# Kernel tuning notes

Hardware: AMD Instinct MI355X
Metric: run time of the kernel (lower is better)

Reference implementation:

```python
import jax, jax.numpy as jnp
import numpy as np
import math

B = 8
LATENT = 1024
K_DIM = 128   # conv input channels / view dim k
M_DIM = 256   # attention feature dim m
N = 4096      # points_num // num_branch; attention seq len
EPS = 1e-5


def _bn(h, g, b, m, v):
    # inference-mode BatchNorm1d over [B, C, L]
    return (h - m[None, :, None]) * (g / jnp.sqrt(v + EPS))[None, :, None] + b[None, :, None]


def _conv(h, w, b):
    # Conv1d with kernel_size=1 == channel matmul: h [B,C,L], w [O,C]
    return jnp.einsum('bcl,oc->bol', h, w) + b[None, :, None]


def setup_inputs() -> dict:
    key = jax.random.key(0)
    ks = jax.random.split(key, 64)
    it = iter(range(64))

    def nrm(shape, scale=0.05):
        return jax.random.normal(ks[next(it)], shape, jnp.float32) * scale

    def pos(shape):
        return jax.random.uniform(ks[next(it)], shape, jnp.float32, 0.5, 1.5)

    d = {}
    d['x'] = jax.random.normal(ks[next(it)], (B, LATENT), jnp.float32)
    d['fc1_w'] = nrm((M_DIM * K_DIM, LATENT))
    d['fc1_b'] = nrm((M_DIM * K_DIM,))
    d['c1q_w'] = nrm((64, K_DIM)); d['c1q_b'] = nrm((64,))
    d['c2q_w'] = nrm((128, 64));   d['c2q_b'] = nrm((128,))
    d['c3q_w'] = nrm((N, 128));    d['c3q_b'] = nrm((N,))
    d['c3k_w'] = nrm((N, 128));    d['c3k_b'] = nrm((N,))
    d['c1v_w'] = nrm((64, K_DIM)); d['c1v_b'] = nrm((64,))
    d['c2v_w'] = nrm((128, 64));   d['c2v_b'] = nrm((128,))
    d['c3v_w'] = nrm((N, 128));    d['c3v_b'] = nrm((N,))
    for nm, c in [('bn1q', 64), ('bn2q', 128), ('bn1k', 64), ('bn2k', 128), ('bn1v', 64), ('bn2v', 128)]:
        d[nm + '_g'] = pos((c,))
        d[nm + '_be'] = nrm((c,))
        d[nm + '_m'] = nrm((c,))
        d[nm + '_v'] = pos((c,))
    d['co_w'] = nrm((3, M_DIM)); d['co_b'] = nrm((3,))
    return d


def _forward(x, fc1_w, fc1_b, c1q_w, c1q_b, c2q_w, c2q_b, c3q_w, c3q_b, c3k_w, c3k_b,
             c1v_w, c1v_b, c2v_w, c2v_b, c3v_w, c3v_b,
             bn1q_g, bn1q_be, bn1q_m, bn1q_v, bn2q_g, bn2q_be, bn2q_m, bn2q_v,
             bn1k_g, bn1k_be, bn1k_m, bn1k_v, bn2k_g, bn2k_be, bn2k_m, bn2k_v,
             bn1v_g, bn1v_be, bn1v_m, bn1v_v, bn2v_g, bn2v_be, bn2v_m, bn2v_v,
             co_w, co_b):
    h = (x @ fc1_w.T + fc1_b).reshape(-1, M_DIM, K_DIM)   # [B, m, k]
    h = jnp.transpose(h, (0, 2, 1))                        # [B, k, m]
    # Q path
    Q = jax.nn.relu(_bn(_conv(h, c1q_w, c1q_b), bn1q_g, bn1q_be, bn1q_m, bn1q_v))
    Q = jax.nn.relu(_bn(_conv(Q, c2q_w, c2q_b), bn2q_g, bn2q_be, bn2q_m, bn2q_v))
    Q = _conv(Q, c3q_w, c3q_b)                             # [B, n, m]
    # K path: source re-uses conv1_q / conv2_q weights (faithful to original)
    K = jax.nn.relu(_bn(_conv(h, c1q_w, c1q_b), bn1k_g, bn1k_be, bn1k_m, bn1k_v))
    K = jax.nn.relu(_bn(_conv(K, c2q_w, c2q_b), bn2k_g, bn2k_be, bn2k_m, bn2k_v))
    K = _conv(K, c3k_w, c3k_b)                             # [B, n, m]
    # V path
    V = jax.nn.relu(_bn(_conv(h, c1v_w, c1v_b), bn1v_g, bn1v_be, bn1v_m, bn1v_v))
    V = jax.nn.relu(_bn(_conv(V, c2v_w, c2v_b), bn2v_g, bn2v_be, bn2v_m, bn2v_v))
    V = _conv(V, c3v_w, c3v_b)                             # [B, n, m]
    # hand-rolled attention: scores [B, n, n] (source scales by sqrt(k))
    scores = jnp.einsum('bim,bjm->bij', Q, K) / math.sqrt(K_DIM)
    attn = jax.nn.softmax(scores, axis=2)
    out = jnp.einsum('bij,bjm->bim', attn, V)              # [B, n, m]
    out = jnp.einsum('bnm,om->bon', out, co_w) + co_b[None, :, None]  # [B, 3, n]
    return jnp.transpose(out, (0, 2, 1))                   # [B, n, 3]


def reference(x, fc1_w, fc1_b, c1q_w, c1q_b, c2q_w, c2q_b, c3q_w, c3q_b, c3k_w, c3k_b,
              c1v_w, c1v_b, c2v_w, c2v_b, c3v_w, c3v_b,
              bn1q_g, bn1q_be, bn1q_m, bn1q_v, bn2q_g, bn2q_be, bn2q_m, bn2q_v,
              bn1k_g, bn1k_be, bn1k_m, bn1k_v, bn2k_g, bn2k_be, bn2k_m, bn2k_v,
              bn1v_g, bn1v_be, bn1v_m, bn1v_v, bn2v_g, bn2v_be, bn2v_m, bn2v_v,
              co_w, co_b):
    return _forward(x, fc1_w, fc1_b, c1q_w, c1q_b, c2q_w, c2q_b, c3q_w, c3q_b, c3k_w, c3k_b,
                    c1v_w, c1v_b, c2v_w, c2v_b, c3v_w, c3v_b,
                    bn1q_g, bn1q_be, bn1q_m, bn1q_v, bn2q_g, bn2q_be, bn2q_m, bn2q_v,
                    bn1k_g, bn1k_be, bn1k_m, bn1k_v, bn2k_g, bn2k_be, bn2k_m, bn2k_v,
                    bn1v_g, bn1v_be, bn1v_m, bn1v_v, bn2v_g, bn2v_be, bn2v_m, bn2v_v,
                    co_w, co_b)
```

## Files before the change

### kernel.cpp

```cpp
#include <hip/hip_runtime.h>
#include <cstdint>
#include <cstddef>

#define EPS 1e-5f

typedef __attribute__((ext_vector_type(8))) short bf16x8;
typedef __attribute__((ext_vector_type(4))) float f32x4;
typedef __attribute__((ext_vector_type(16))) float f32x16;

__device__ __forceinline__ unsigned short rne_bf16(float f) {
  union { float f; unsigned int u; } v; v.f = f;
  unsigned int u = v.u;
  return (unsigned short)((u + 0x7fffu + ((u >> 16) & 1u)) >> 16);
}
__device__ __forceinline__ float bf16_to_f(unsigned short h) {
  union { unsigned int u; float f; } v; v.u = ((unsigned int)h) << 16; return v.f;
}
__device__ __forceinline__ void split_hl(float v, unsigned short& h, unsigned short& l) {
  h = rne_bf16(v);
  l = rne_bf16(v - bf16_to_f(h));
}
__device__ __forceinline__ f32x4 mfma16(bf16x8 a, bf16x8 b, f32x4 c) {
  return __builtin_amdgcn_mfma_f32_16x16x32_bf16(a, b, c, 0, 0, 0);
}
__device__ __forceinline__ f32x16 mfma32(bf16x8 a, bf16x8 b, f32x16 c) {
  return __builtin_amdgcn_mfma_f32_32x32x16_bf16(a, b, c, 0, 0, 0);
}

__global__ __launch_bounds__(256) void k_fc1(const float* __restrict__ x,
                                             const float* __restrict__ w,
                                             const float* __restrict__ bias,
                                             float* __restrict__ h_t) {
  const int lane = threadIdx.x & 63;
  const int wv = threadIdx.x >> 6;
  const int r = blockIdx.x * 4 + wv;
  const float4* wr = (const float4*)(w + (size_t)r * 1024);
  float acc[8] = {0, 0, 0, 0, 0, 0, 0, 0};
#pragma unroll
  for (int i = 0; i < 4; ++i) {
    float4 wv4 = wr[lane + i * 64];
#pragma unroll
    for (int b = 0; b < 8; ++b) {
      float4 xv = ((const float4*)(x + b * 1024))[lane + i * 64];
      acc[b] += wv4.x * xv.x + wv4.y * xv.y + wv4.z * xv.z + wv4.w * xv.w;
    }
  }
#pragma unroll
  for (int d = 1; d < 64; d <<= 1) {
#pragma unroll
    for (int b = 0; b < 8; ++b) acc[b] += __shfl_xor(acc[b], d);
  }
  if (lane == 0) {
    const int mm = r >> 7, kk = r & 127;
    const float bb = bias[r];
#pragma unroll
    for (int b = 0; b < 8; ++b) h_t[b * 32768 + kk * 256 + mm] = acc[b] + bb;
  }
}

__global__ __launch_bounds__(256) void k_conv1(
    const float* __restrict__ h_t,
    const float* __restrict__ c1q_w, const float* __restrict__ c1q_b,
    const float* __restrict__ c1v_w, const float* __restrict__ c1v_b,
    const float* __restrict__ g1q, const float* __restrict__ be1q,
    const float* __restrict__ mu1q, const float* __restrict__ va1q,
    const float* __restrict__ g1k, const float* __restrict__ be1k,
    const float* __restrict__ mu1k, const float* __restrict__ va1k,
    const float* __restrict__ g1v, const float* __restrict__ be1v,
    const float* __restrict__ mu1v, const float* __restrict__ va1v,
    float* __restrict__ T1q, float* __restrict__ T1k, float* __restrict__ T1v) {
  const int m = threadIdx.x;
  const int o = blockIdx.x & 63;
  const int b = blockIdx.x >> 6;
  const int path = blockIdx.y;
  const float* w = (path == 0 ? c1q_w : c1v_w) + o * 128;
  const float* h = h_t + b * 32768 + m;
  float acc = 0.f;
#pragma unroll 8
  for (int c = 0; c < 128; ++c) acc += w[c] * h[c * 256];
  if (path == 0) {
    const float z = acc + c1q_b[o];
    const float sq = g1q[o] / sqrtf(va1q[o] + EPS);
    T1q[b * 16384 + o * 256 + m] = fmaxf((z - mu1q[o]) * sq + be1q[o], 0.f);
    const float sk = g1k[o] / sqrtf(va1k[o] + EPS);
    T1k[b * 16384 + o * 256 + m] = fmaxf((z - mu1k[o]) * sk + be1k[o], 0.f);
  } else {
    const float z = acc + c1v_b[o];
    const float sv = g1v[o] / sqrtf(va1v[o] + EPS);
    T1v[b * 16384 + o * 256 + m] = fmaxf((z - mu1v[o]) * sv + be1v[o], 0.f);
  }
}

__global__ __launch_bounds__(256) void k_conv2(
    const float* __restrict__ T1q, const float* __restrict__ T1k,
    const float* __restrict__ T1v,
    const float* __restrict__ c2q_w, const float* __restrict__ c2q_b,
    const float* __restrict__ c2v_w, const float* __restrict__ c2v_b,
    const float* __restrict__ g2q, const float* __restrict__ be2q,
    const float* __restrict__ mu2q, const float* __restrict__ va2q,
    const float* __restrict__ g2k, const float* __restrict__ be2k,
    const float* __restrict__ mu2k, const float* __restrict__ va2k,
    const float* __restrict__ g2v, const float* __restrict__ be2v,
    const float* __restrict__ mu2v, const float* __restrict__ va2v,
    unsigned short* __restrict__ Q2H, unsigned short* __restrict__ Q2L,
    unsigned short* __restrict__ K2H, unsigned short* __restrict__ K2L,
    float* __restrict__ V2F) {
  const int m = threadIdx.x;
  const int b = blockIdx.x;
  const int path = blockIdx.y;
  const int oc = blockIdx.z;
  const float* T1 = (path == 0 ? T1q : path == 1 ? T1k : T1v) + b * 16384 + m;
  const float* w = (path == 2 ? c2v_w : c2q_w);
  const float* cb = (path == 2 ? c2v_b : c2q_b);
  const float* g = (path == 0 ? g2q : path == 1 ? g2k : g2v);
  const float* be = (path == 0 ? be2q : path == 1 ? be2k : be2v);
  const float* mu = (path == 0 ? mu2q : path == 1 ? mu2k : mu2v);
  const float* va = (path == 0 ? va2q : path == 1 ? va2k : va2v);
  float t[64];
#pragma unroll
  for (int c = 0; c < 64; ++c) t[c] = T1[c * 256];
  unsigned short* oh =
      (path == 0 ? Q2H : K2H) + b * 32768 + m * 128 + oc * 64;
  unsigned short* ol =
      (path == 0 ? Q2L : K2L) + b * 32768 + m * 128 + oc * 64;
  for (int og = 0; og < 8; ++og) {
    bf16x8 ph, pl;
#pragma unroll
    for (int j = 0; j < 8; ++j) {
      const int o = oc * 64 + og * 8 + j;
      float acc = cb[o];
      const float* wo = w + o * 64;
#pragma unroll
      for (int c = 0; c < 64; ++c) acc += wo[c] * t[c];
      const float s = g[o] / sqrtf(va[o] + EPS);
      const float val = fmaxf((acc - mu[o]) * s + be[o], 0.f);
      if (path == 2) {
        V2F[b * 32768 + o * 256 + m] = val;
      } else {
        unsigned short hh, ll;
        split_hl(val, hh, ll);
        ph[j] = (short)hh; pl[j] = (short)ll;
      }
    }
    if (path != 2) {
      *(bf16x8*)(oh + og * 8) = ph;
      *(bf16x8*)(ol + og * 8) = pl;
    }
  }
}

__global__ __launch_bounds__(256) void k_conv3all(
    const float* __restrict__ c3q_w, const float* __restrict__ c3q_b,
    const float* __restrict__ c3k_w, const float* __restrict__ c3k_b,
    const unsigned short* __restrict__ Q2H, const unsigned short* __restrict__ Q2L,
    const unsigned short* __restrict__ K2H, const unsigned short* __restrict__ K2L,
    unsigned short* __restrict__ QhB, unsigned short* __restrict__ QlB,
    unsigned short* __restrict__ KhB, unsigned short* __restrict__ KlB,
    const float* __restrict__ c3v_w, const float* __restrict__ c3v_b,
    const float* __restrict__ V2F, const float* __restrict__ co_w,
    float4* __restrict__ Vpp) {
  const int z = blockIdx.z;
  const int b = blockIdx.y;
  if (z == 2) {
    if (blockIdx.x >= 16) return;
    __shared__ float Us[387];
    __shared__ float Up[256][3];
    const int tt = threadIdx.x;
    {
      const int c = tt >> 1, mh = tt & 1;
      const float* v = V2F + b * 32768 + c * 256 + mh * 128;
      const float* cw0 = co_w + mh * 128;
      float u0 = 0.f, u1 = 0.f, u2 = 0.f;
#pragma unroll 4
      for (int mm = 0; mm < 128; ++mm) {
        const float xv = v[mm];
        u0 += xv * cw0[mm];
        u1 += xv * cw0[256 + mm];
        u2 += xv * cw0[512 + mm];
      }
      Up[tt][0] = u0; Up[tt][1] = u1; Up[tt][2] = u2;
      if (tt < 3) {
        float s = 0.f;
        for (int mm = 0; mm < 256; ++mm) s += co_w[tt * 256 + mm];
        Us[384 + tt] = s;
      }
    }
    __syncthreads();
    if ((tt & 1) == 0) {
      const int c = tt >> 1;
      Us[c * 3 + 0] = Up[tt][0] + Up[tt + 1][0];
      Us[c * 3 + 1] = Up[tt][1] + Up[tt + 1][1];
      Us[c * 3 + 2] = Up[tt][2] + Up[tt + 1][2];
    }
    __syncthreads();
    const int n = blockIdx.x * 256 + tt;
    const float* w = c3v_w + (size_t)n * 128;
    float a0 = 0.f, a1 = 0.f, a2 = 0.f;
#pragma unroll 4
    for (int c = 0; c < 128; ++c) {
      const float wc = w[c];
      a0 += wc * Us[c * 3 + 0];
      a1 += wc * Us[c * 3 + 1];
      a2 += wc * Us[c * 3 + 2];
    }
    const float bb = c3v_b[n];
    Vpp[(size_t)b * 4096 + n] =
        make_float4(a0 + bb * Us[384], a1 + bb * Us[385], a2 + bb * Us[386], 0.f);
    return;
  }
  const float* W = (z == 0) ? c3q_w : c3k_w;
  const float* bias = (z == 0) ? c3q_b : c3k_b;
  const unsigned short* Xh = (z == 0) ? Q2H : K2H;
  const unsigned short* Xl = (z == 0) ? Q2L : K2L;
  unsigned short* Yh = (z == 0) ? QhB : KhB;
  unsigned short* Yl = (z == 0) ? QlB : KlB;
  const float scale = (z == 0) ? 0.08838834764831845f * 1.4426950408889634f : 1.0f;
  const int lane = threadIdx.x & 63, wv = threadIdx.x >> 6;
  const int l15 = lane & 15, quad = lane >> 4;
  const unsigned short* XH = Xh + b * 32768;
  const unsigned short* XL = Xl + b * 32768;
  unsigned short* YH = Yh + (size_t)b * 4096 * 256;
  unsigned short* YL = Yl + (size_t)b * 4096 * 256;
  const int nb = blockIdx.x * 64 + wv * 16;
  const float* wr = W + (size_t)(nb + l15) * 128 + quad * 8;
  bf16x8 ah[4], al[4];
#pragma unroll
  for (int ks = 0; ks < 4; ++ks) {
#pragma unroll
    for (int j = 0; j < 8; ++j) {
      unsigned short hh, ll;
      split_hl(wr[ks * 32 + j], hh, ll);
      ah[ks][j] = (short)hh; al[ks][j] = (short)ll;
    }
  }
  f32x4 acc[16];
#pragma unroll
  for (int ms = 0; ms < 16; ++ms) acc[ms] = (f32x4){0, 0, 0, 0};
#pragma unroll
  for (int ks = 0; ks < 4; ++ks) {
#pragma unroll
    for (int ms = 0; ms < 16; ++ms) {
      const size_t off = (size_t)(ms * 16 + l15) * 128 + ks * 32 + quad * 8;
      bf16x8 bh = *(const bf16x8*)(XH + off);
      bf16x8 bl = *(const bf16x8*)(XL + off);
      acc[ms] = mfma16(ah[ks], bh, acc[ms]);
      acc[ms] = mfma16(al[ks], bh, acc[ms]);
      acc[ms] = mfma16(ah[ks], bl, acc[ms]);
    }
  }
#pragma unroll
  for (int r = 0; r < 4; ++r) {
    const int n = nb + quad * 4 + r;
    const float bv = bias[n];
#pragma unroll
    for (int ms = 0; ms < 16; ++ms) {
      const float v = (acc[ms][r] + bv) * scale;
      unsigned short hh, ll;
      split_hl(v, hh, ll);
      YH[(size_t)n * 256 + ms * 16 + l15] = hh;
      YL[(size_t)n * 256 + ms * 16 + l15] = ll;
    }
  }
}

__global__ __launch_bounds__(256, 2) void k_attn(
    const unsigned short* __restrict__ Qh, const unsigned short* __restrict__ Ql,
    const unsigned short* __restrict__ Kh, const unsigned short* __restrict__ Kl,
    const float4* __restrict__ Vpp, float* __restrict__ partsum,
    unsigned int* __restrict__ cnt, const float* __restrict__ co_b,
    float* __restrict__ out) {
  __shared__ __align__(16) short Kt[2][2][32 * 264];
  __shared__ __align__(16) float4 Vt[2][32];
  const int t = threadIdx.x;
  const int lane = t & 63, wv = t >> 6;
  const int l31 = lane & 31, half = lane >> 5;
  const int b = blockIdx.x & 7;
  const int qt = (blockIdx.x >> 3) & 31;
  const int jh = blockIdx.x >> 8;
  const int qrow = qt * 128 + wv * 32 + l31;
  const size_t qoff = ((size_t)b * 4096 + qrow) * 256 + half * 8;
  bf16x8 qfh[16], qfl[16];
#pragma unroll
  for (int kc = 0; kc < 16; ++kc) {
    qfh[kc] = *(const bf16x8*)(Qh + qoff + kc * 16);
    qfl[kc] = *(const bf16x8*)(Ql + qoff + kc * 16);
  }
  const unsigned short* Kgh = Kh + (size_t)b * 4096 * 256;
  const unsigned short* Kgl = Kl + (size_t)b * 4096 * 256;
  const float4* Vg = Vpp + (size_t)b * 4096;
  const int r0 = t >> 5;
  const int sseg = (t & 31) * 8;
  float a0 = 0.f, a1 = 0.f, a2 = 0.f, al = 0.f;
  const int jt0 = jh * 64;
  {
    const int jbase = jt0 * 32;
#pragma unroll
    for (int i = 0; i < 4; ++i) {
      const int row = i * 8 + r0;
      const size_t g = (size_t)(jbase + row) * 256 + sseg;
      *(bf16x8*)&Kt[0][0][row * 264 + sseg] = *(const bf16x8*)(Kgh + g);
      *(bf16x8*)&Kt[0][1][row * 264 + sseg] = *(const bf16x8*)(Kgl + g);
    }
    if (t < 32) Vt[0][t] = Vg[jbase + t];
  }
  __syncthreads();
  for (int it = 0; it < 64; ++it) {
    const int cur = it & 1, nxt = cur ^ 1;
    const bool pf = (it < 63);
    bf16x8 th[4], tl[4];
    float4 vpf = make_float4(0.f, 0.f, 0.f, 0.f);
    if (pf) {
      const int jb2 = (jt0 + it + 1) * 32;
#pragma unroll
      for (int i = 0; i < 4; ++i) {
        const size_t g = (size_t)(jb2 + i * 8 + r0) * 256 + sseg;
        th[i] = *(const bf16x8*)(Kgh + g);
        tl[i] = *(const bf16x8*)(Kgl + g);
      }
      if (t < 32) vpf = Vg[jb2 + t];
    }
    f32x16 sA, sB, sC;
#pragma unroll
    for (int r = 0; r < 16; ++r) { sA[r] = 0.f; sB[r] = 0.f; sC[r] = 0.f; }
    const short* KH = Kt[cur][0];
    const short* KL = Kt[cur][1];
    __builtin_amdgcn_s_setprio(1);
#pragma unroll
    for (int kc = 0; kc < 16; ++kc) {
      bf16x8 kh = *(const bf16x8*)&KH[l31 * 264 + kc * 16 + half * 8];
      bf16x8 kl = *(const bf16x8*)&KL[l31 * 264 + kc * 16 + half * 8];
      sA = mfma32(kh, qfh[kc], sA);
      sB = mfma32(kh, qfl[kc], sB);
      sC = mfma32(kl, qfh[kc], sC);
    }
    __builtin_amdgcn_s_setprio(0);
#pragma unroll
    for (int r = 0; r < 16; ++r) {
      const float p = __builtin_amdgcn_exp2f(sA[r] + sB[r] + sC[r]);
      const float4 vj = Vt[cur][(r & 3) + 8 * (r >> 2) + 4 * half];
      a0 += p * vj.x; a1 += p * vj.y; a2 += p * vj.z; al += p;
    }
    if (pf) {
#pragma unroll
      for (int i = 0; i < 4; ++i) {
        const int row = i * 8 + r0;
        *(bf16x8*)&Kt[nxt][0][row * 264 + sseg] = th[i];
        *(bf16x8*)&Kt[nxt][1][row * 264 + sseg] = tl[i];
      }
      if (t < 32) Vt[nxt][t] = vpf;
    }
    __syncthreads();
  }
  a0 += __shfl_xor(a0, 32);
  a1 += __shfl_xor(a1, 32);
  a2 += __shfl_xor(a2, 32);
  al += __shfl_xor(al, 32);
  if (half == 0) {
    const int idx = b * 4096 + qrow;
    float* ps = partsum + (size_t)idx * 4;
    atomicAdd(ps + 0, a0);
    atomicAdd(ps + 1, a1);
    atomicAdd(ps + 2, a2);
    atomicAdd(ps + 3, al);
    __threadfence();
    const unsigned int old = atomicAdd(&cnt[idx], 1u);
    if (old == 1u) {
      const float s0 = atomicAdd(ps + 0, 0.f);
      const float s1 = atomicAdd(ps + 1, 0.f);
      const float s2 = atomicAdd(ps + 2, 0.f);
      const float sl = atomicAdd(ps + 3, 0.f);
      const float rl = 1.f / sl;
      out[(size_t)idx * 3 + 0] = s0 * rl + co_b[0];
      out[(size_t)idx * 3 + 1] = s1 * rl + co_b[1];
      out[(size_t)idx * 3 + 2] = s2 * rl + co_b[2];
    }
  }
}

extern "C" void kernel_launch(void* const* d_in, const int* in_sizes, int n_in,
                              void* d_out, int out_size, void* d_ws, size_t ws_size,
                              hipStream_t stream) {
  const float* x = (const float*)d_in[0];
  const float* fc1_w = (const float*)d_in[1];
  const float* fc1_b = (const float*)d_in[2];
  const float* c1q_w = (const float*)d_in[3];
  const float* c1q_b = (const float*)d_in[4];
  const float* c2q_w = (const float*)d_in[5];
  const float* c2q_b = (const float*)d_in[6];
  const float* c3q_w = (const float*)d_in[7];
  const float* c3q_b = (const float*)d_in[8];
  const float* c3k_w = (const float*)d_in[9];
  const float* c3k_b = (const float*)d_in[10];
  const float* c1v_w = (const float*)d_in[11];
  const float* c1v_b = (const float*)d_in[12];
  const float* c2v_w = (const float*)d_in[13];
  const float* c2v_b = (const float*)d_in[14];
  const float* c3v_w = (const float*)d_in[15];
  const float* c3v_b = (const float*)d_in[16];
  const float* bn1q_g = (const float*)d_in[17];
  const float* bn1q_be = (const float*)d_in[18];
  const float* bn1q_m = (const float*)d_in[19];
  const float* bn1q_v = (const float*)d_in[20];
  const float* bn2q_g = (const float*)d_in[21];
  const float* bn2q_be = (const float*)d_in[22];
  const float* bn2q_m = (const float*)d_in[23];
  const float* bn2q_v = (const float*)d_in[24];
  const float* bn1k_g = (const float*)d_in[25];
  const float* bn1k_be = (const float*)d_in[26];
  const float* bn1k_m = (const float*)d_in[27];
  const float* bn1k_v = (const float*)d_in[28];
  const float* bn2k_g = (const float*)d_in[29];
  const float* bn2k_be = (const float*)d_in[30];
  const float* bn2k_m = (const float*)d_in[31];
  const float* bn2k_v = (const float*)d_in[32];
  const float* bn1v_g = (const float*)d_in[33];
  const float* bn1v_be = (const float*)d_in[34];
  const float* bn1v_m = (const float*)d_in[35];
  const float* bn1v_v = (const float*)d_in[36];
  const float* bn2v_g = (const float*)d_in[37];
  const float* bn2v_be = (const float*)d_in[38];
  const float* bn2v_m = (const float*)d_in[39];
  const float* bn2v_v = (const float*)d_in[40];
  const float* co_w = (const float*)d_in[41];
  const float* co_b = (const float*)d_in[42];

  char* ws = (char*)d_ws;
  float* h_t = (float*)(ws + 0);
  float* T1q = (float*)(ws + 1048576);
  float* T1k = (float*)(ws + 1572864);
  float* T1v = (float*)(ws + 2097152);
  unsigned short* Q2H = (unsigned short*)(ws + 2621440);
  unsigned short* Q2L = (unsigned short*)(ws + 3145728);
  unsigned short* K2H = (unsigned short*)(ws + 3670016);
  unsigned short* K2L = (unsigned short*)(ws + 4194304);
  float* V2F = (float*)(ws + 4718592);
  unsigned short* QhB = (unsigned short*)(ws + 5767168);
  unsigned short* QlB = (unsigned short*)(ws + 22544384);
  unsigned short* KhB = (unsigned short*)(ws + 39321600);
  unsigned short* KlB = (unsigned short*)(ws + 56098816);
  float4* Vpp = (float4*)(ws + 72876032);
  float* partsum = (float*)(ws + 73416704);
  unsigned int* cnt = (unsigned int*)(ws + 73940992);

  hipMemsetAsync(ws + 73416704, 0, 524288 + 131072, stream);

  k_fc1<<<8192, 256, 0, stream>>>(x, fc1_w, fc1_b, h_t);
  k_conv1<<<dim3(512, 2), 256, 0, stream>>>(
      h_t, c1q_w, c1q_b, c1v_w, c1v_b,
      bn1q_g, bn1q_be, bn1q_m, bn1q_v,
      bn1k_g, bn1k_be, bn1k_m, bn1k_v,
      bn1v_g, bn1v_be, bn1v_m, bn1v_v,
      T1q, T1k, T1v);
  k_conv2<<<dim3(8, 3, 2), 256, 0, stream>>>(
      T1q, T1k, T1v, c2q_w, c2q_b, c2v_w, c2v_b,
      bn2q_g, bn2q_be, bn2q_m, bn2q_v,
      bn2k_g, bn2k_be, bn2k_m, bn2k_v,
      bn2v_g, bn2v_be, bn2v_m, bn2v_v,
      Q2H, Q2L, K2H, K2L, V2F);
  k_conv3all<<<dim3(64, 8, 3), 256, 0, stream>>>(
      c3q_w, c3q_b, c3k_w, c3k_b, Q2H, Q2L, K2H, K2L,
      QhB, QlB, KhB, KlB, c3v_w, c3v_b, V2F, co_w, Vpp);
  k_attn<<<512, 256, 0, stream>>>(QhB, QlB, KhB, KlB, Vpp, partsum, cnt,
                                  co_b, (float*)d_out);
}
```

Before: 707.0 us.

## Process two query subtiles per wave in attention to reuse K tiles

Each wave in the attention kernel now handles 64 query rows (two 32-row subtiles) instead of 32, so every K tile loaded from LDS feeds twice as many MFMAs. The grid is halved to 256 blocks and launch bounds drop to one block per CU. LDS double buffering is replaced by a single buffer with an extra barrier before overwriting it. This raises register pressure, lowers occupancy to 256 blocks, and serialises the K tile handoff between iterations.

```diff
diff --git a/kernel.cpp b/kernel.cpp
--- a/kernel.cpp
+++ b/kernel.cpp
@@ -263,116 +263,129 @@
   }
 }
 
-__global__ __launch_bounds__(256, 2) void k_attn(
+__global__ __launch_bounds__(256, 1) void k_attn(
     const unsigned short* __restrict__ Qh, const unsigned short* __restrict__ Ql,
     const unsigned short* __restrict__ Kh, const unsigned short* __restrict__ Kl,
     const float4* __restrict__ Vpp, float* __restrict__ partsum,
     unsigned int* __restrict__ cnt, const float* __restrict__ co_b,
     float* __restrict__ out) {
-  __shared__ __align__(16) short Kt[2][2][32 * 264];
-  __shared__ __align__(16) float4 Vt[2][32];
+  __shared__ __align__(16) short Kth[32 * 264];
+  __shared__ __align__(16) short Ktl[32 * 264];
+  __shared__ __align__(16) float4 Vt[32];
   const int t = threadIdx.x;
   const int lane = t & 63, wv = t >> 6;
   const int l31 = lane & 31, half = lane >> 5;
   const int b = blockIdx.x & 7;
-  const int qt = (blockIdx.x >> 3) & 31;
-  const int jh = blockIdx.x >> 8;
-  const int qrow = qt * 128 + wv * 32 + l31;
-  const size_t qoff = ((size_t)b * 4096 + qrow) * 256 + half * 8;
-  bf16x8 qfh[16], qfl[16];
+  const int qt = (blockIdx.x >> 3) & 15;
+  const int jh = blockIdx.x >> 7;
+  const int qbase = qt * 256 + wv * 64;
+  const size_t qoff0 = ((size_t)b * 4096 + qbase + l31) * 256 + half * 8;
+  const size_t qoff1 = qoff0 + 32 * 256;
+  bf16x8 qh0[16], ql0[16], qh1[16], ql1[16];
 #pragma unroll
   for (int kc = 0; kc < 16; ++kc) {
-    qfh[kc] = *(const bf16x8*)(Qh + qoff + kc * 16);
-    qfl[kc] = *(const bf16x8*)(Ql + qoff + kc * 16);
+    qh0[kc] = *(const bf16x8*)(Qh + qoff0 + kc * 16);
+    ql0[kc] = *(const bf16x8*)(Ql + qoff0 + kc * 16);
+    qh1[kc] = *(const bf16x8*)(Qh + qoff1 + kc * 16);
+    ql1[kc] = *(const bf16x8*)(Ql + qoff1 + kc * 16);
   }
   const unsigned short* Kgh = Kh + (size_t)b * 4096 * 256;
   const unsigned short* Kgl = Kl + (size_t)b * 4096 * 256;
   const float4* Vg = Vpp + (size_t)b * 4096;
-  const int r0 = t >> 5;
+  const int rr = t >> 5;
   const int sseg = (t & 31) * 8;
-  float a0 = 0.f, a1 = 0.f, a2 = 0.f, al = 0.f;
-  const int jt0 = jh * 64;
+  float a00 = 0.f, a01 = 0.f, a02 = 0.f, a0l = 0.f;
+  float a10 = 0.f, a11 = 0.f, a12 = 0.f, a1l = 0.f;
+  const int jrow0 = jh * 2048;
   {
-    const int jbase = jt0 * 32;
 #pragma unroll
     for (int i = 0; i < 4; ++i) {
-      const int row = i * 8 + r0;
-      const size_t g = (size_t)(jbase + row) * 256 + sseg;
-      *(bf16x8*)&Kt[0][0][row * 264 + sseg] = *(const bf16x8*)(Kgh + g);
-      *(bf16x8*)&Kt[0][1][row * 264 + sseg] = *(const bf16x8*)(Kgl + g);
-    }
-    if (t < 32) Vt[0][t] = Vg[jbase + t];
+      const int row = i * 8 + rr;
+      const size_t g = (size_t)(jrow0 + row) * 256 + sseg;
+      *(bf16x8*)&Kth[row * 264 + sseg] = *(const bf16x8*)(Kgh + g);
+      *(bf16x8*)&Ktl[row * 264 + sseg] = *(const bf16x8*)(Kgl + g);
+    }
+    if (t < 32) Vt[t] = Vg[jrow0 + t];
   }
   __syncthreads();
   for (int it = 0; it < 64; ++it) {
-    const int cur = it & 1, nxt = cur ^ 1;
     const bool pf = (it < 63);
     bf16x8 th[4], tl[4];
     float4 vpf = make_float4(0.f, 0.f, 0.f, 0.f);
     if (pf) {
-      const int jb2 = (jt0 + it + 1) * 32;
+      const int jb2 = jrow0 + (it + 1) * 32;
 #pragma unroll
       for (int i = 0; i < 4; ++i) {
-        const size_t g = (size_t)(jb2 + i * 8 + r0) * 256 + sseg;
+        const size_t g = (size_t)(jb2 + i * 8 + rr) * 256 + sseg;
         th[i] = *(const bf16x8*)(Kgh + g);
         tl[i] = *(const bf16x8*)(Kgl + g);
       }
       if (t < 32) vpf = Vg[jb2 + t];
     }
-    f32x16 sA, sB, sC;
-#pragma unroll
-    for (int r = 0; r < 16; ++r) { sA[r] = 0.f; sB[r] = 0.f; sC[r] = 0.f; }
-    const short* KH = Kt[cur][0];
-    const short* KL = Kt[cur][1];
-    __builtin_amdgcn_s_setprio(1);
+    f32x16 sA0, sB0, sC0, sA1, sB1, sC1;
+#pragma unroll
+    for (int r = 0; r < 16; ++r) {
+      sA0[r] = 0.f; sB0[r] = 0.f; sC0[r] = 0.f;
+      sA1[r] = 0.f; sB1[r] = 0.f; sC1[r] = 0.f;
+    }
 #pragma unroll
     for (int kc = 0; kc < 16; ++kc) {
-      bf16x8 kh = *(const bf16x8*)&KH[l31 * 264 + kc * 16 + half * 8];
-      bf16x8 kl = *(const bf16x8*)&KL[l31 * 264 + kc * 16 + half * 8];
-      sA = mfma32(kh, qfh[kc], sA);
-      sB = mfma32(kh, qfl[kc], sB);
-      sC = mfma32(kl, qfh[kc], sC);
-    }
-    __builtin_amdgcn_s_setprio(0);
+      bf16x8 kh = *(const bf16x8*)&Kth[l31 * 264 + kc * 16 + half * 8];
+      bf16x8 kl = *(const bf16x8*)&Ktl[l31 * 264 + kc * 16 + half * 8];
+      sA0 = mfma32(kh, qh0[kc], sA0);
+      sA1 = mfma32(kh, qh1[kc], sA1);
+      sB0 = mfma32(kh, ql0[kc], sB0);
+      sB1 = mfma32(kh, ql1[kc], sB1);
+      sC0 = mfma32(kl, qh0[kc], sC0);
+      sC1 = mfma32(kl, qh1[kc], sC1);
+    }
 #pragma unroll
     for (int r = 0; r < 16; ++r) {
-      const float p = __builtin_amdgcn_exp2f(sA[r] + sB[r] + sC[r]);
-      const float4 vj = Vt[cur][(r & 3) + 8 * (r >> 2) + 4 * half];
-      a0 += p * vj.x; a1 += p * vj.y; a2 += p * vj.z; al += p;
-    }
+      const float4 vj = Vt[(r & 3) + 8 * (r >> 2) + 4 * half];
+      const float p0 = __builtin_amdgcn_exp2f(sA0[r] + sB0[r] + sC0[r]);
+      const float p1 = __builtin_amdgcn_exp2f(sA1[r] + sB1[r] + sC1[r]);
+      a00 += p0 * vj.x; a01 += p0 * vj.y; a02 += p0 * vj.z; a0l += p0;
+      a10 += p1 * vj.x; a11 += p1 * vj.y; a12 += p1 * vj.z; a1l += p1;
+    }
+    __syncthreads();
     if (pf) {
 #pragma unroll
       for (int i = 0; i < 4; ++i) {
-        const int row = i * 8 + r0;
-        *(bf16x8*)&Kt[nxt][0][row * 264 + sseg] = th[i];
-        *(bf16x8*)&Kt[nxt][1][row * 264 + sseg] = tl[i];
-      }
-      if (t < 32) Vt[nxt][t] = vpf;
+        const int row = i * 8 + rr;
+        *(bf16x8*)&Kth[row * 264 + sseg] = th[i];
+        *(bf16x8*)&Ktl[row * 264 + sseg] = tl[i];
+      }
+      if (t < 32) Vt[t] = vpf;
     }
     __syncthreads();
   }
-  a0 += __shfl_xor(a0, 32);
-  a1 += __shfl_xor(a1, 32);
-  a2 += __shfl_xor(a2, 32);
-  al += __shfl_xor(al, 32);
+  a00 += __shfl_xor(a00, 32); a01 += __shfl_xor(a01, 32);
+  a02 += __shfl_xor(a02, 32); a0l += __shfl_xor(a0l, 32);
+  a10 += __shfl_xor(a10, 32); a11 += __shfl_xor(a11, 32);
+  a12 += __shfl_xor(a12, 32); a1l += __shfl_xor(a1l, 32);
   if (half == 0) {
-    const int idx = b * 4096 + qrow;
-    float* ps = partsum + (size_t)idx * 4;
-    atomicAdd(ps + 0, a0);
-    atomicAdd(ps + 1, a1);
-    atomicAdd(ps + 2, a2);
-    atomicAdd(ps + 3, al);
-    __threadfence();
-    const unsigned int old = atomicAdd(&cnt[idx], 1u);
-    if (old == 1u) {
-      const float s0 = atomicAdd(ps + 0, 0.f);
-      const float s1 = atomicAdd(ps + 1, 0.f);
-      const float s2 = atomicAdd(ps + 2, 0.f);
-      const float sl = atomicAdd(ps + 3, 0.f);
-      const float rl = 1.f / sl;
-      out[(size_t)idx * 3 + 0] = s0 * rl + co_b[0];
-      out[(size_t)idx * 3 + 1] = s1 * rl + co_b[1];
-      out[(size_t)idx * 3 + 2] = s2 * rl + co_b[2];
+#pragma unroll
+    for (int s = 0; s < 2; ++s) {
+      const float v0 = s ? a10 : a00, v1 = s ? a11 : a01;
+      const float v2 = s ? a12 : a02, vl = s ? a1l : a0l;
+      const int idx = b * 4096 + qbase + s * 32 + l31;
+      float* ps = partsum + (size_t)idx * 4;
+      atomicAdd(ps + 0, v0);
+      atomicAdd(ps + 1, v1);
+      atomicAdd(ps + 2, v2);
+      atomicAdd(ps + 3, vl);
+      __threadfence();
+      const unsigned int old = atomicAdd(&cnt[idx], 1u);
+      if (old == 1u) {
+        const float s0 = atomicAdd(ps + 0, 0.f);
+        const float s1 = atomicAdd(ps + 1, 0.f);
+        const float s2 = atomicAdd(ps + 2, 0.f);
+        const float sl = atomicAdd(ps + 3, 0.f);
+        const float rl = 1.f / sl;
+        out[(size_t)idx * 3 + 0] = s0 * rl + co_b[0];
+        out[(size_t)idx * 3 + 1] = s1 * rl + co_b[1];
+        out[(size_t)idx * 3 + 2] = s2 * rl + co_b[2];
+      }
     }
   }
 }
@@ -460,6 +473,6 @@
   k_conv3all<<<dim3(64, 8, 3), 256, 0, stream>>>(
       c3q_w, c3q_b, c3k_w, c3k_b, Q2H, Q2L, K2H, K2L,
       QhB, QlB, KhB, KlB, c3v_w, c3v_b, V2F, co_w, Vpp);
-  k_attn<<<512, 256, 0, stream>>>(QhB, QlB, KhB, KlB, Vpp, partsum, cnt,
+  k_attn<<<256, 256, 0, stream>>>(QhB, QlB, KhB, KlB, Vpp, partsum, cnt,
                                   co_b, (float*)d_out);
 }
```

Result: faster. 676.4 us (-4.3%).
